# Kernel optimization log

Hardware: AMD Instinct MI355X
Metric: run time of the kernel (lower is better)

The kernel has to match this reference:

```python
import jax, jax.numpy as jnp
import numpy as np

NUM_HEADS = 16


def setup_inputs() -> dict:
    key = jax.random.key(0)
    ks = jax.random.split(key, 8)
    B, S, E = 2, 2048, 1024
    w_scale = 0.02  # xavier-ish init scale
    return {
        "x": jax.random.normal(ks[0], (B, S, E), dtype=jnp.float32),
        "qkv_w": jax.random.normal(ks[1], (3 * E, E), dtype=jnp.float32) * w_scale,
        "qkv_b": jnp.zeros((3 * E,), dtype=jnp.float32),
        "out_w": jax.random.normal(ks[2], (E, E), dtype=jnp.float32) * w_scale,
        "out_b": jnp.zeros((E,), dtype=jnp.float32),
        "head_gates": jax.random.normal(ks[3], (NUM_HEADS,), dtype=jnp.float32) + 1.0,
        "head_importance": jax.random.normal(ks[4], (NUM_HEADS,), dtype=jnp.float32) + 1.0,
        "head_threshold": jax.random.uniform(ks[5], (), dtype=jnp.float32),
    }


def reference(x, qkv_w, qkv_b, out_w, out_b, head_gates, head_importance, head_threshold):
    B, S, E = x.shape
    H = NUM_HEADS
    D = E // H
    # dynamic head selection: gate score vs learned threshold -> binary per-head mask
    gate_score = jax.nn.sigmoid(head_gates * head_importance)          # [H]
    active_heads = (gate_score > head_threshold).astype(x.dtype)       # [H]

    qkv = x @ qkv_w.T + qkv_b                                          # [B,S,3E]
    qkv = qkv.reshape(B, S, 3, H, D).transpose(2, 0, 3, 1, 4)          # [3,B,H,S,D]
    qkv = qkv * active_heads[None, None, :, None, None]                # mask inactive heads
    q, k, v = qkv[0], qkv[1], qkv[2]

    # NOTE: source computes scale = sqrt(head_dim) but never applies it -> unscaled scores
    scores = jnp.einsum('bhsd,bhtd->bhst', q, k)                       # [B,H,S,S]
    attn = jax.nn.softmax(scores, axis=-1)
    out = jnp.einsum('bhst,bhtd->bhsd', attn, v)
    out = out + v.mean(axis=2, keepdims=True)                          # residual mean of v over seq

    out = out.transpose(0, 2, 1, 3).reshape(B, S, E)
    return out @ out_w.T + out_b
```

## Files before the change

kernel.cpp:

```cpp
#include <hip/hip_runtime.h>

#define BB 2
#define SS 2048
#define EE 1024
#define HH 16
#define DD_ 64
#define BH (BB*HH)
#define NQKV (3*EE)
#define MROWS (BB*SS)

typedef _Float16 f16;
typedef _Float16 f16x8 __attribute__((ext_vector_type(8)));
typedef _Float16 f16x4 __attribute__((ext_vector_type(4)));
typedef __fp16 fp16x2 __attribute__((ext_vector_type(2)));
typedef float f32x4 __attribute__((ext_vector_type(4)));
typedef float f32x16 __attribute__((ext_vector_type(16)));

#define MFMA16(a,b,c) __builtin_amdgcn_mfma_f32_16x16x32_f16(a,b,c,0,0,0)
#define MFMA32(a,b,c) __builtin_amdgcn_mfma_f32_32x32x16_f16(a,b,c,0,0,0)
#define EXP2F(x) __builtin_amdgcn_exp2f(x)
#define LOG2E 1.44269504088896f

__device__ __forceinline__ bool head_active(
    const float* gates, const float* imp, const float* thr, int h) {
    const float gs = 1.f / (1.f + __expf(-gates[h] * imp[h]));
    return gs > thr[0];
}

__device__ __forceinline__ void gload16(const void* g, void* l) {
    __builtin_amdgcn_global_load_lds(
        (const __attribute__((address_space(1))) void*)g,
        (__attribute__((address_space(3))) void*)l, 16, 0, 0);
}

__device__ __forceinline__ float vmax16(f32x16 v) {
    float a = fmaxf(v[0], v[1]),  b = fmaxf(v[2], v[3]);
    float c = fmaxf(v[4], v[5]),  d = fmaxf(v[6], v[7]);
    float e = fmaxf(v[8], v[9]),  f = fmaxf(v[10], v[11]);
    float g = fmaxf(v[12], v[13]), h = fmaxf(v[14], v[15]);
    a = fmaxf(a, b); c = fmaxf(c, d); e = fmaxf(e, f); g = fmaxf(g, h);
    return fmaxf(fmaxf(a, c), fmaxf(e, g));
}

#define NX4  1048576
#define NW14  786432
#define NW24  262144
__global__ __launch_bounds__(256) void cvt_kernel(
    const float* __restrict__ x, const float* __restrict__ w1,
    const float* __restrict__ w2, f16* __restrict__ x16,
    f16* __restrict__ w116, f16* __restrict__ w216,
    const float* __restrict__ gates, const float* __restrict__ imp,
    const float* __restrict__ thr)
{
    const int i = blockIdx.x * 256 + threadIdx.x;
    const float* src; f16* dst; int off;
    if (i < NX4)              { src = x;  dst = x16;  off = i; }
    else if (i < NX4 + NW14)  {
        src = w1; dst = w116; off = i - NX4;
        const int row = off >> 8;
        if (!head_active(gates, imp, thr, (row & 1023) >> 6)) return;
    }
    else                      { src = w2; dst = w216; off = i - NX4 - NW14; }
    float4 v = ((const float4*)src)[off];
    f16x4 h = { (f16)v.x, (f16)v.y, (f16)v.z, (f16)v.w };
    *(f16x4*)(dst + 4*(size_t)off) = h;
}

__global__ __launch_bounds__(256) void qkv_gemm_kernel(
    const f16* __restrict__ x, const f16* __restrict__ w,
    const float* __restrict__ bias, const float* __restrict__ gates,
    const float* __restrict__ imp, const float* __restrict__ thr,
    f16* __restrict__ q16, f16* __restrict__ k16, f16* __restrict__ v16)
{
    __shared__ f16 As[2][128*64];
    __shared__ f16 Bs[2][64*64];
    const int tid  = threadIdx.x;
    const int wave = tid >> 6, lane = tid & 63;
    const int quad = lane >> 4, l15 = lane & 15;
    const int m0 = blockIdx.x << 7;
    const int n0 = blockIdx.y << 6;
    const int which = n0 >> 10;
    const int h     = (n0 & 1023) >> 6;
    if (!head_active(gates, imp, thr, h)) return;

#define QSTAGE(K0, B) do {                                                   \
    _Pragma("unroll")                                                        \
    for (int u = 0; u < 4; ++u) {                                            \
        const int s_ = tid + (u << 8);                                       \
        const int r_ = s_ >> 3;                                              \
        const int sc_ = ((s_ & 7) ^ (r_ & 7)) << 3;                          \
        gload16(x + (size_t)(m0 + r_)*EE + (K0) + sc_, &As[B][s_ << 3]);     \
    }                                                                        \
    _Pragma("unroll")                                                        \
    for (int u = 0; u < 2; ++u) {                                            \
        const int s_ = tid + (u << 8);                                       \
        const int r_ = s_ >> 3;                                              \
        const int sc_ = ((s_ & 7) ^ (r_ & 7)) << 3;                          \
        gload16(w + (size_t)(n0 + r_)*EE + (K0) + sc_, &Bs[B][s_ << 3]);     \
    } } while (0)

    f32x4 acc[2][4];
#pragma unroll
    for (int i = 0; i < 2; ++i)
#pragma unroll
        for (int j = 0; j < 4; ++j) acc[i][j] = (f32x4){0.f,0.f,0.f,0.f};

    QSTAGE(0, 0);
    int cur = 0;
    for (int t = 0; t < 16; ++t) {
        __syncthreads();
        if (t < 15) QSTAGE((t + 1) << 6, cur ^ 1);
#pragma unroll
        for (int ks = 0; ks < 2; ++ks) {
            f16x8 af[2], bf[4];
#pragma unroll
            for (int i = 0; i < 2; ++i) {
                const int r = wave*32 + i*16 + l15;
                af[i] = *(const f16x8*)&As[cur][(r << 6) + ((((ks<<2)+quad) ^ (l15 & 7)) << 3)];
            }
#pragma unroll
            for (int j = 0; j < 4; ++j) {
                const int r = j*16 + l15;
                bf[j] = *(const f16x8*)&Bs[cur][(r << 6) + ((((ks<<2)+quad) ^ (l15 & 7)) << 3)];
            }
#pragma unroll
            for (int i = 0; i < 2; ++i)
#pragma unroll
                for (int j = 0; j < 4; ++j)
                    acc[i][j] = MFMA16(af[i], bf[j], acc[i][j]);
        }
        cur ^= 1;
    }
#undef QSTAGE

    const float scale = (which == 0) ? LOG2E : 1.f;
    f16* __restrict__ dst = (which == 0) ? q16 : ((which == 1) ? k16 : v16);
    float bv[4];
#pragma unroll
    for (int j = 0; j < 4; ++j) bv[j] = bias[n0 + j*16 + l15];
#pragma unroll
    for (int i = 0; i < 2; ++i) {
#pragma unroll
        for (int reg = 0; reg < 4; ++reg) {
            const int m = m0 + wave*32 + i*16 + quad*4 + reg;
            const int b = m >> 11, s = m & (SS - 1);
            f16* rowp = dst + (((size_t)(b*HH + h))*SS + s)*DD_ + l15;
#pragma unroll
            for (int j = 0; j < 4; ++j)
                rowp[j*16] = (f16)((acc[i][j][reg] + bv[j]) * scale);
        }
    }
}

__global__ __launch_bounds__(256) void vtrans_kernel(
    const f16* __restrict__ v16, f16* __restrict__ vt, float* __restrict__ vmean,
    const float* __restrict__ gates, const float* __restrict__ imp,
    const float* __restrict__ thr)
{
    const int bh = blockIdx.y;
    if (!head_active(gates, imp, thr, bh & (HH - 1))) return;
    __shared__ f16 T[64][74];
    const int tid = threadIdx.x;
    const int s0 = blockIdx.x << 6;
#pragma unroll
    for (int u = 0; u < 2; ++u) {
        const int f = tid + (u << 8);
        const int r = f >> 3, c = (f & 7) << 3;
        *(f16x8*)&T[r][c] = *(const f16x8*)(v16 + ((size_t)bh*SS + s0 + r)*DD_ + c);
    }
    __syncthreads();
    const int d = tid >> 2, ch = (tid & 3) << 4;
    union { f16 h[16]; f16x8 v8[2]; } t;
    float ps = 0.f;
#pragma unroll
    for (int u = 0; u < 16; ++u) { f16 val = T[ch + u][d]; t.h[u] = val; ps += (float)val; }
    f16* dp = vt + ((size_t)bh*DD_ + d)*SS + s0 + ch;
    *(f16x8*)(dp)     = t.v8[0];
    *(f16x8*)(dp + 8) = t.v8[1];
    ps += __shfl_xor(ps, 1, 64);
    ps += __shfl_xor(ps, 2, 64);
    if ((tid & 3) == 0) atomicAdd(vmean + bh*DD_ + d, ps * (1.f / SS));
}

template<int KPL>
__global__ __launch_bounds__(256, 4) void attn_kernel(
    const f16* __restrict__ q16, const f16* __restrict__ k16,
    const f16* __restrict__ vt,
    const float* __restrict__ gates, const float* __restrict__ imp,
    const float* __restrict__ thr,
    float* __restrict__ opart, float* __restrict__ mlpart)
{
    constexpr int NT = 1 << (5 - KPL);
    __shared__ f16 Ks[2][64*64];
    __shared__ f16 Vs[2][64*64];
    const int tid  = threadIdx.x;
    const int wave = tid >> 6, lane = tid & 63;
    const int l31 = lane & 31, hi = lane >> 5, l7 = lane & 7;
    const int bh = blockIdx.y;
    const int kp = blockIdx.x & ((1 << KPL) - 1);
    const int qc = blockIdx.x >> KPL;
    const int q0 = qc << 7;
    const int k0 = kp << (11 - KPL);

    if (!head_active(gates, imp, thr, bh & (HH - 1))) return;

    const f16* qb = q16 + (size_t)bh * SS * DD_;
    const f16* kb = k16 + (size_t)bh * SS * DD_;
    const f16* vb = vt  + (size_t)bh * DD_ * SS;

    const int r0 = tid >> 3, r1 = r0 + 32, cc = tid & 7;
    const int sc0 = (cc ^ (r0 & 7)) << 3;
    const int sc1 = (cc ^ (r1 & 7)) << 3;

    gload16(kb + (size_t)(k0 + r0)*DD_ + sc0, &Ks[0][tid << 3]);
    gload16(kb + (size_t)(k0 + r1)*DD_ + sc1, &Ks[0][(tid + 256) << 3]);
    gload16(vb + (size_t)r0*SS + k0 + sc0,    &Vs[0][tid << 3]);
    gload16(vb + (size_t)r1*SS + k0 + sc1,    &Vs[0][(tid + 256) << 3]);

    f16x8 qf[4];
#pragma unroll
    for (int ks = 0; ks < 4; ++ks)
        qf[ks] = *(const f16x8*)(qb +
            (size_t)(q0 + wave*32 + l31)*DD_ + ks*16 + hi*8);

    f32x16 accO[2];
#pragma unroll
    for (int dt = 0; dt < 2; ++dt)
#pragma unroll
        for (int r = 0; r < 16; ++r) accO[dt][r] = 0.f;
    float M = 0.f;
    float lsum = 0.f;

    int cur = 0;
    for (int t = 0; t < NT; ++t) {
        const int kt = k0 + (t << 6);
        __syncthreads();
        if (t < NT - 1) {
            const int kn = kt + 64;
            gload16(kb + (size_t)(kn + r0)*DD_ + sc0, &Ks[cur^1][tid << 3]);
            gload16(kb + (size_t)(kn + r1)*DD_ + sc1, &Ks[cur^1][(tid + 256) << 3]);
            gload16(vb + (size_t)r0*SS + kn + sc0,    &Vs[cur^1][tid << 3]);
            gload16(vb + (size_t)r1*SS + kn + sc1,    &Vs[cur^1][(tid + 256) << 3]);
        }

        f32x16 accS[2];
        const float negM = -M;
#pragma unroll
        for (int mt = 0; mt < 2; ++mt)
#pragma unroll
            for (int r = 0; r < 16; ++r) accS[mt][r] = negM;
        __builtin_amdgcn_s_setprio(1);
#pragma unroll
        for (int ks = 0; ks < 4; ++ks)
#pragma unroll
            for (int mt = 0; mt < 2; ++mt) {
                f16x8 kf = *(const f16x8*)&Ks[cur][((mt*32 + l31) << 6) +
                                                  ((((ks<<1)+hi) ^ l7) << 3)];
                accS[mt] = MFMA32(kf, qf[ks], accS[mt]);
            }
        __builtin_amdgcn_s_setprio(0);

        const float mxl = fmaxf(vmax16(accS[0]), vmax16(accS[1]));
        if (!__all(mxl <= 8.f)) {
            float mx = mxl;
            mx = fmaxf(mx, __shfl_xor(mx, 1, 64));
            mx = fmaxf(mx, __shfl_xor(mx, 2, 64));
            mx = fmaxf(mx, __shfl_xor(mx, 4, 64));
            mx = fmaxf(mx, __shfl_xor(mx, 8, 64));
            mx = fmaxf(mx, __shfl_xor(mx, 16, 64));
            mx = fmaxf(mx, __shfl_xor(mx, 32, 64));
            const float alpha = EXP2F(-mx);
            M += mx;
            lsum *= alpha;
#pragma unroll
            for (int r = 0; r < 16; ++r) { accO[0][r] *= alpha; accO[1][r] *= alpha; }
#pragma unroll
            for (int mt = 0; mt < 2; ++mt)
#pragma unroll
                for (int r = 0; r < 16; ++r) accS[mt][r] -= mx;
        }

        float rs[2];
#pragma unroll
        for (int mt = 0; mt < 2; ++mt) {
            float t0 = 0.f, t1 = 0.f, t2 = 0.f, t3 = 0.f;
#pragma unroll
            for (int r = 0; r < 16; r += 4) {
                float p0 = EXP2F(accS[mt][r+0]); accS[mt][r+0] = p0; t0 += p0;
                float p1 = EXP2F(accS[mt][r+1]); accS[mt][r+1] = p1; t1 += p1;
                float p2 = EXP2F(accS[mt][r+2]); accS[mt][r+2] = p2; t2 += p2;
                float p3 = EXP2F(accS[mt][r+3]); accS[mt][r+3] = p3; t3 += p3;
            }
            rs[mt] = (t0 + t1) + (t2 + t3);
        }
        float sum = rs[0] + rs[1];
        sum += __shfl_xor(sum, 32, 64);
        lsum += sum;

        int pki[2][8];
#pragma unroll
        for (int mt = 0; mt < 2; ++mt)
#pragma unroll
            for (int t2_ = 0; t2_ < 8; ++t2_) {
                union { fp16x2 h; int i; } c;
                c.h = __builtin_amdgcn_cvt_pkrtz(accS[mt][2*t2_], accS[mt][2*t2_+1]);
                pki[mt][t2_] = c.i;
            }

#pragma unroll
        for (int ks = 0; ks < 4; ++ks) {
            const int mt = ks >> 1;
            const int bidx = (ks & 1) << 2;
            const int a0 = pki[mt][bidx+0], a1 = pki[mt][bidx+1];
            const int b0 = pki[mt][bidx+2], b1 = pki[mt][bidx+3];
            const int s0 = hi ? a0 : b0;
            const int s1 = hi ? a1 : b1;
            const int r0x = __shfl_xor(s0, 32, 64);
            const int r1x = __shfl_xor(s1, 32, 64);
            union { int i[4]; f16x8 h; } u;
            u.i[0] = hi ? r0x : a0;
            u.i[1] = hi ? r1x : a1;
            u.i[2] = hi ? b0 : r0x;
            u.i[3] = hi ? b1 : r1x;
            f16x8 pf = u.h;
            __builtin_amdgcn_s_setprio(1);
#pragma unroll
            for (int dt = 0; dt < 2; ++dt) {
                f16x8 vf = *(const f16x8*)&Vs[cur][((dt*32 + l31) << 6) +
                                                  ((((ks<<1)+hi) ^ l7) << 3)];
                accO[dt] = MFMA32(vf, pf, accO[dt]);
            }
            __builtin_amdgcn_s_setprio(0);
        }
        cur ^= 1;
    }

    {
        const int s = q0 + wave*32 + l31;
        const size_t rowi = (size_t)kp*BH*SS + (size_t)bh*SS + s;
        float* ob = opart + (rowi << 6);
#pragma unroll
        for (int dt = 0; dt < 2; ++dt)
#pragma unroll
            for (int g = 0; g < 4; ++g) {
                const int d0 = dt*32 + 8*g + 4*hi;
                float4 o = { accO[dt][4*g+0], accO[dt][4*g+1],
                             accO[dt][4*g+2], accO[dt][4*g+3] };
                *(float4*)(ob + d0) = o;
            }
        if (hi == 0) {
            float2 ml = { M, lsum };
            *(float2*)(mlpart + rowi*2) = ml;
        }
    }
}

template<int PARTS>
__global__ __launch_bounds__(256) void combine_kernel(
    const float* __restrict__ opart, const float* __restrict__ mlpart,
    const float* __restrict__ vmean,
    const float* __restrict__ gates, const float* __restrict__ imp,
    const float* __restrict__ thr, f16* __restrict__ aout)
{
    const int t = blockIdx.x * 256 + threadIdx.x;
    const int row = t >> 2;
    const int dc = (t & 3) << 4;
    const int bh = row >> 11, s = row & (SS - 1);
    const int b = bh >> 4, h = bh & (HH - 1);

    if (!head_active(gates, imp, thr, h)) return;

    f16* op = aout + ((size_t)(b*SS + s))*EE + h*DD_ + dc;
    float2 ml[PARTS];
    float mx = -1.0e30f;
#pragma unroll
    for (int p = 0; p < PARTS; ++p) {
        ml[p] = ((const float2*)mlpart)[(size_t)p*BH*SS + row];
        mx = fmaxf(mx, ml[p].x);
    }
    float a[PARTS], denom = 0.f;
#pragma unroll
    for (int p = 0; p < PARTS; ++p) {
        a[p] = EXP2F(ml[p].x - mx);
        denom += ml[p].y * a[p];
    }
    const float inv = 1.f / denom;
    const float* o0 = opart + ((size_t)row << 6) + dc;
#pragma unroll
    for (int j = 0; j < 4; ++j) {
        float4 acc = {0.f, 0.f, 0.f, 0.f};
#pragma unroll
        for (int p = 0; p < PARTS; ++p) {
            float4 v = ((const float4*)(o0 + (size_t)p*BH*SS*DD_))[j];
            acc.x += v.x*a[p]; acc.y += v.y*a[p];
            acc.z += v.z*a[p]; acc.w += v.w*a[p];
        }
        float4 vm = *(const float4*)(vmean + bh*DD_ + dc + 4*j);
        f16x4 o = { (f16)(acc.x*inv + vm.x), (f16)(acc.y*inv + vm.y),
                    (f16)(acc.z*inv + vm.z), (f16)(acc.w*inv + vm.w) };
        *(f16x4*)(op + 4*j) = o;
    }
}

__global__ __launch_bounds__(256) void out_gemm_kernel(
    const f16* __restrict__ a, const f16* __restrict__ w,
    const float* __restrict__ bias, const float* __restrict__ gates,
    const float* __restrict__ imp, const float* __restrict__ thr,
    float* __restrict__ y)
{
    __shared__ f16 As[2][128*64];
    __shared__ f16 Bs[2][128*64];
    const int tid  = threadIdx.x;
    const int wave = tid >> 6, lane = tid & 63;
    const int quad = lane >> 4, l15 = lane & 15;
    const int wm = wave & 1, wn = wave >> 1;
    const int m0 = blockIdx.y << 7, n0 = blockIdx.x << 7;

    unsigned hmask = 0;
#pragma unroll
    for (int h = 0; h < HH; ++h)
        if (head_active(gates, imp, thr, h)) hmask |= (1u << h);

#define OSTAGE(K0, B) do {                                                   \
    _Pragma("unroll")                                                        \
    for (int u = 0; u < 4; ++u) {                                            \
        const int s_ = tid + (u << 8);                                       \
        const int r_ = s_ >> 3;                                              \
        const int sc_ = ((s_ & 7) ^ (r_ & 7)) << 3;                          \
        gload16(a + (size_t)(m0 + r_)*EE + (K0) + sc_, &As[B][s_ << 3]);     \
        gload16(w + (size_t)(n0 + r_)*EE + (K0) + sc_, &Bs[B][s_ << 3]);     \
    } } while (0)

    f32x4 acc[4][4];
#pragma unroll
    for (int i = 0; i < 4; ++i)
#pragma unroll
        for (int j = 0; j < 4; ++j) acc[i][j] = (f32x4){0.f,0.f,0.f,0.f};

    unsigned m = hmask;
    int kcur = m ? (__ffs(m) - 1) : -1;
    if (m) m &= m - 1;
    if (kcur >= 0) OSTAGE(kcur << 6, 0);
    int cur = 0;
    while (kcur >= 0) {
        const int knext = m ? (__ffs(m) - 1) : -1;
        if (m) m &= m - 1;
        __syncthreads();
        if (knext >= 0) OSTAGE(knext << 6, cur ^ 1);
#pragma unroll
        for (int ks = 0; ks < 2; ++ks) {
            f16x8 af[4], bf[4];
#pragma unroll
            for (int i = 0; i < 4; ++i) {
                const int r = wm*64 + i*16 + l15;
                af[i] = *(const f16x8*)&As[cur][(r << 6) + ((((ks<<2)+quad) ^ (l15 & 7)) << 3)];
            }
#pragma unroll
            for (int j = 0; j < 4; ++j) {
                const int r = wn*64 + j*16 + l15;
                bf[j] = *(const f16x8*)&Bs[cur][(r << 6) + ((((ks<<2)+quad) ^ (l15 & 7)) << 3)];
            }
#pragma unroll
            for (int i = 0; i < 4; ++i)
#pragma unroll
                for (int j = 0; j < 4; ++j)
                    acc[i][j] = MFMA16(af[i], bf[j], acc[i][j]);
        }
        cur ^= 1;
        kcur = knext;
    }
#undef OSTAGE

    float bv[4];
#pragma unroll
    for (int j = 0; j < 4; ++j) bv[j] = bias[n0 + wn*64 + j*16 + l15];
#pragma unroll
    for (int i = 0; i < 4; ++i) {
#pragma unroll
        for (int reg = 0; reg < 4; ++reg) {
            const int m2 = m0 + wm*64 + i*16 + quad*4 + reg;
#pragma unroll
            for (int j = 0; j < 4; ++j)
                y[(size_t)m2*EE + n0 + wn*64 + j*16 + l15] = acc[i][j][reg] + bv[j];
        }
    }
}

extern "C" void kernel_launch(void* const* d_in, const int* in_sizes, int n_in,
                              void* d_out, int out_size, void* d_ws, size_t ws_size,
                              hipStream_t stream)
{
    const float* x      = (const float*)d_in[0];
    const float* qkv_w  = (const float*)d_in[1];
    const float* qkv_b  = (const float*)d_in[2];
    const float* out_w  = (const float*)d_in[3];
    const float* out_b  = (const float*)d_in[4];
    const float* gates  = (const float*)d_in[5];
    const float* imp    = (const float*)d_in[6];
    const float* thr    = (const float*)d_in[7];
    float* out = (float*)d_out;

    const size_t TSZ = (size_t)BH * SS * DD_;
    f16* x16  = (f16*)d_ws;
    f16* w116 = x16 + (size_t)MROWS * EE;
    f16* w216 = w116 + (size_t)NQKV * EE;
    f16* q16  = w216 + (size_t)EE * EE;
    f16* k16  = q16 + TSZ;
    f16* v16  = k16 + TSZ;
    f16* vtb  = v16 + TSZ;
    f16* aout = vtb + TSZ;
    float* vmean  = (float*)(aout + TSZ);
    float* opart  = vmean + (size_t)BH * DD_;

    const size_t base_bytes = (size_t)((char*)opart - (char*)d_ws);
    const size_t per_part   = (size_t)BH*SS*DD_*4 + (size_t)BH*SS*2*4;
    const int parts = (ws_size >= base_bytes + 4*per_part) ? 4 : 2;

    float* mlpart = opart + (size_t)parts*BH*SS*DD_;

    (void)hipMemsetAsync(vmean, 0, (size_t)BH * DD_ * sizeof(float), stream);

    cvt_kernel<<<(NX4 + NW14 + NW24) / 256, 256, 0, stream>>>(
        x, qkv_w, out_w, x16, w116, w216, gates, imp, thr);

    dim3 g1(MROWS/128, NQKV/64);
    qkv_gemm_kernel<<<g1, 256, 0, stream>>>(x16, w116, qkv_b, gates, imp, thr,
                                            q16, k16, v16);
    dim3 g2(SS/64, BH);
    vtrans_kernel<<<g2, 256, 0, stream>>>(v16, vtb, vmean, gates, imp, thr);

    dim3 g2a(16 * parts, BH);
    if (parts == 4)
        attn_kernel<2><<<g2a, 256, 0, stream>>>(q16, k16, vtb, gates, imp, thr,
                                                opart, mlpart);
    else
        attn_kernel<1><<<g2a, 256, 0, stream>>>(q16, k16, vtb, gates, imp, thr,
                                                opart, mlpart);

    if (parts == 4)
        combine_kernel<4><<<(BH*SS*4)/256, 256, 0, stream>>>(
            opart, mlpart, vmean, gates, imp, thr, aout);
    else
        combine_kernel<2><<<(BH*SS*4)/256, 256, 0, stream>>>(
            opart, mlpart, vmean, gates, imp, thr, aout);

    dim3 g3(EE/128, MROWS/128);
    out_gemm_kernel<<<g3, 256, 0, stream>>>(aout, w216, out_b, gates, imp, thr,
                                            out);
}
```

Baseline: 162.6 us.

## Fuse V transpose and mean into QKV GEMM epilogue, drop memset

The QKV GEMM epilogue now writes the V projection directly in transposed [bh][d][s] layout and accumulates the per-column V sums into vmean via shuffles and atomics, removing the separate vtrans kernel and its round trip through an intermediate V buffer. Zeroing of vmean moves into block 0 of the conversion kernel, replacing a hipMemsetAsync launch. The transposed stores are 4-element f16 writes strided by SS, so they are less coalesced than the old row-major writes, and there are more atomics per vmean element.

```diff
diff --git a/kernel.cpp b/kernel.cpp
--- a/kernel.cpp
+++ b/kernel.cpp
@@ -50,8 +50,13 @@
     const float* __restrict__ w2, f16* __restrict__ x16,
     f16* __restrict__ w116, f16* __restrict__ w216,
     const float* __restrict__ gates, const float* __restrict__ imp,
-    const float* __restrict__ thr)
+    const float* __restrict__ thr, float* __restrict__ vmean)
 {
+    if (blockIdx.x == 0) {
+        const float4 z = {0.f, 0.f, 0.f, 0.f};
+        ((float4*)vmean)[threadIdx.x*2]     = z;
+        ((float4*)vmean)[threadIdx.x*2 + 1] = z;
+    }
     const int i = blockIdx.x * 256 + threadIdx.x;
     const float* src; f16* dst; int off;
     if (i < NX4)              { src = x;  dst = x16;  off = i; }
@@ -70,7 +75,8 @@
     const f16* __restrict__ x, const f16* __restrict__ w,
     const float* __restrict__ bias, const float* __restrict__ gates,
     const float* __restrict__ imp, const float* __restrict__ thr,
-    f16* __restrict__ q16, f16* __restrict__ k16, f16* __restrict__ v16)
+    f16* __restrict__ q16, f16* __restrict__ k16,
+    f16* __restrict__ vtb, float* __restrict__ vmean)
 {
     __shared__ f16 As[2][128*64];
     __shared__ f16 Bs[2][64*64];
@@ -133,11 +139,44 @@
     }
 #undef QSTAGE
 
+    float bv[4];
+#pragma unroll
+    for (int j = 0; j < 4; ++j) bv[j] = bias[n0 + j*16 + l15];
+
+    if (which == 2) {
+        const int b  = m0 >> 11, s0 = m0 & (SS - 1);
+        const int bh = b*HH + h;
+        f16* vt_base = vtb + ((size_t)bh * DD_) * SS + s0;
+        float colsum[4];
+#pragma unroll
+        for (int j = 0; j < 4; ++j) {
+            colsum[j] = 0.f;
+#pragma unroll
+            for (int i = 0; i < 2; ++i) {
+                f16x4 pk;
+#pragma unroll
+                for (int reg = 0; reg < 4; ++reg) {
+                    const f16 hv = (f16)(acc[i][j][reg] + bv[j]);
+                    pk[reg] = hv;
+                    colsum[j] += (float)hv;
+                }
+                const int m_loc = wave*32 + i*16 + quad*4;
+                *(f16x4*)(vt_base + (size_t)(j*16 + l15)*SS + m_loc) = pk;
+            }
+        }
+#pragma unroll
+        for (int j = 0; j < 4; ++j) {
+            float c = colsum[j];
+            c += __shfl_xor(c, 16, 64);
+            c += __shfl_xor(c, 32, 64);
+            if (quad == 0)
+                atomicAdd(vmean + bh*DD_ + j*16 + l15, c * (1.f / SS));
+        }
+        return;
+    }
+
     const float scale = (which == 0) ? LOG2E : 1.f;
-    f16* __restrict__ dst = (which == 0) ? q16 : ((which == 1) ? k16 : v16);
-    float bv[4];
-#pragma unroll
-    for (int j = 0; j < 4; ++j) bv[j] = bias[n0 + j*16 + l15];
+    f16* __restrict__ dst = (which == 0) ? q16 : k16;
 #pragma unroll
     for (int i = 0; i < 2; ++i) {
 #pragma unroll
@@ -150,36 +189,6 @@
                 rowp[j*16] = (f16)((acc[i][j][reg] + bv[j]) * scale);
         }
     }
-}
-
-__global__ __launch_bounds__(256) void vtrans_kernel(
-    const f16* __restrict__ v16, f16* __restrict__ vt, float* __restrict__ vmean,
-    const float* __restrict__ gates, const float* __restrict__ imp,
-    const float* __restrict__ thr)
-{
-    const int bh = blockIdx.y;
-    if (!head_active(gates, imp, thr, bh & (HH - 1))) return;
-    __shared__ f16 T[64][74];
-    const int tid = threadIdx.x;
-    const int s0 = blockIdx.x << 6;
-#pragma unroll
-    for (int u = 0; u < 2; ++u) {
-        const int f = tid + (u << 8);
-        const int r = f >> 3, c = (f & 7) << 3;
-        *(f16x8*)&T[r][c] = *(const f16x8*)(v16 + ((size_t)bh*SS + s0 + r)*DD_ + c);
-    }
-    __syncthreads();
-    const int d = tid >> 2, ch = (tid & 3) << 4;
-    union { f16 h[16]; f16x8 v8[2]; } t;
-    float ps = 0.f;
-#pragma unroll
-    for (int u = 0; u < 16; ++u) { f16 val = T[ch + u][d]; t.h[u] = val; ps += (float)val; }
-    f16* dp = vt + ((size_t)bh*DD_ + d)*SS + s0 + ch;
-    *(f16x8*)(dp)     = t.v8[0];
-    *(f16x8*)(dp + 8) = t.v8[1];
-    ps += __shfl_xor(ps, 1, 64);
-    ps += __shfl_xor(ps, 2, 64);
-    if ((tid & 3) == 0) atomicAdd(vmean + bh*DD_ + d, ps * (1.f / SS));
 }
 
 template<int KPL>
@@ -506,8 +515,7 @@
     f16* w216 = w116 + (size_t)NQKV * EE;
     f16* q16  = w216 + (size_t)EE * EE;
     f16* k16  = q16 + TSZ;
-    f16* v16  = k16 + TSZ;
-    f16* vtb  = v16 + TSZ;
+    f16* vtb  = k16 + TSZ;
     f16* aout = vtb + TSZ;
     float* vmean  = (float*)(aout + TSZ);
     float* opart  = vmean + (size_t)BH * DD_;
@@ -518,16 +526,12 @@
 
     float* mlpart = opart + (size_t)parts*BH*SS*DD_;
 
-    (void)hipMemsetAsync(vmean, 0, (size_t)BH * DD_ * sizeof(float), stream);
-
     cvt_kernel<<<(NX4 + NW14 + NW24) / 256, 256, 0, stream>>>(
-        x, qkv_w, out_w, x16, w116, w216, gates, imp, thr);
+        x, qkv_w, out_w, x16, w116, w216, gates, imp, thr, vmean);
 
     dim3 g1(MROWS/128, NQKV/64);
     qkv_gemm_kernel<<<g1, 256, 0, stream>>>(x16, w116, qkv_b, gates, imp, thr,
-                                            q16, k16, v16);
-    dim3 g2(SS/64, BH);
-    vtrans_kernel<<<g2, 256, 0, stream>>>(v16, vtb, vmean, gates, imp, thr);
+                                            q16, k16, vtb, vmean);
 
     dim3 g2a(16 * parts, BH);
     if (parts == 4)
```

Result: no change. 161.4 us (-0.7%).
